# Kernel optimization log

Measured on AMD Instinct MI355X. Metric: run time of the kernel, lower is better.

The kernel has to match this reference:

```python
import jax, jax.numpy as jnp
import numpy as np

NCE_T = 0.07


def setup_inputs() -> dict:
    key = jax.random.key(0)
    k1, k2, k3 = jax.random.split(key, 3)
    features_1 = jax.random.normal(k1, (1, 20000, 256), dtype=jnp.float32)
    features_2 = jax.random.normal(k2, (1, 8192, 256), dtype=jnp.float32)
    map21 = jax.random.randint(k3, (8192,), 0, 20000, dtype=jnp.int64)
    return {"features_1": features_1, "features_2": features_2, "map21": map21}


def reference(features_1, features_2, map21):
    # squeeze leading batch dim (module assumes batch size 1)
    f1 = features_1[0]  # [N1, D]
    f2 = features_2[0]  # [P, D]  (P == nce_num_pairs == len(map21) -> arange branch)
    query = f1[map21]   # [P, D] gather
    keys = f2           # [P, D]
    # pairwise Euclidean distance via matmul trick (matches torch.cdist p=2)
    q_sq = jnp.sum(query * query, axis=-1)  # [P]
    k_sq = jnp.sum(keys * keys, axis=-1)    # [P]
    sq_dist = q_sq[:, None] + k_sq[None, :] - 2.0 * (query @ keys.T)  # [P, P]
    dist = jnp.sqrt(jnp.maximum(sq_dist, 0.0))
    logits = -dist / NCE_T
    # cross entropy with labels = arange(P): mean of -log_softmax diagonal
    logp = jax.nn.log_softmax(logits, axis=-1)
    loss = -jnp.mean(jnp.diagonal(logp))
    return loss
```

## Files before the change

kernel.cpp:

```cpp
#include <hip/hip_runtime.h>
#include <hip/hip_bf16.h>

#define PP      8192
#define DIM     256
#define DIMP    272
#define NKF     17
#define GS      (32 * DIMP)
#define NCHUNK  16
#define TCOLS   16
#define ROWBLK  256
#define NROWBLK (PP / ROWBLK)
#define TILEB   (32 * DIMP * 2)

typedef __bf16 bf16_t;
using bf16x8 = __attribute__((ext_vector_type(8))) __bf16;
using bf16x4 = __attribute__((ext_vector_type(4))) __bf16;
using f32x4  = __attribute__((ext_vector_type(4))) float;
using f32x16 = __attribute__((ext_vector_type(16))) float;

typedef __attribute__((address_space(1))) void as1_void;
typedef __attribute__((address_space(3))) void as3_void;

#define C2    20.609929155556618
#define MEXP  (-340.0f)
#define COEF  ((float)(-(C2 * 1.4142135623730951) * 8388608.0))
#define KBIAS ((float)((127.0 + 340.0) * 8388608.0))
#define LN2   0.6931471805599453f

__global__ __launch_bounds__(256) void nce_prep(
    const float* __restrict__ f1, const float* __restrict__ f2,
    const int* __restrict__ map,
    bf16_t* __restrict__ qb2, bf16_t* __restrict__ kb2,
    float* __restrict__ diag2, float* __restrict__ part_l,
    unsigned* __restrict__ cnt, float* __restrict__ out)
{
    const int tid  = threadIdx.x;
    const int wave = tid >> 6, lane = tid & 63;
    const int p    = blockIdx.x * 4 + wave;
    const int gtid = blockIdx.x * 256 + tid;

    if (gtid < PP) part_l[gtid] = 0.0f;
    if (gtid < NROWBLK) cnt[gtid] = 0u;
    if (gtid == 0) out[0] = 0.0f;

    const int idx = map[p];
    const f32x4 qv = *(const f32x4*)(f1 + (size_t)idx * DIM + lane * 4);
    const f32x4 kv = *(const f32x4*)(f2 + (size_t)p * DIM + lane * 4);

    float qs = qv[0]*qv[0] + qv[1]*qv[1] + qv[2]*qv[2] + qv[3]*qv[3];
    float ks = kv[0]*kv[0] + kv[1]*kv[1] + kv[2]*kv[2] + kv[3]*kv[3];
    const f32x4 dv = qv - kv;
    float ds = dv[0]*dv[0] + dv[1]*dv[1] + dv[2]*dv[2] + dv[3]*dv[3];

    bf16x4 qo, ko;
    #pragma unroll
    for (int i = 0; i < 4; ++i) { qo[i] = (bf16_t)qv[i]; ko[i] = (bf16_t)kv[i]; }

    const int G = p >> 5, l31 = p & 31;
    const int kk = lane >> 2, h = (lane >> 1) & 1, j0 = (lane & 1) * 4;
    const size_t base = (size_t)G * GS;
    const size_t off  = base + (size_t)(kk * 64 + h * 32 + l31) * 8 + j0;
    *(bf16x4*)(qb2 + off) = qo;
    *(bf16x4*)(kb2 + off) = ko;

    #pragma unroll
    for (int s = 32; s > 0; s >>= 1) {
        qs += __shfl_xor(qs, s);
        ks += __shfl_xor(ks, s);
        ds += __shfl_xor(ds, s);
    }

    if (lane < 4) {
        const int hh = lane & 1;
        bf16x8 v;
        #pragma unroll
        for (int i = 0; i < 8; ++i) v[i] = (bf16_t)0.0f;
        if (lane == 0) {
            const float qh = -0.5f * qs;
            const bf16_t q1 = (bf16_t)qh;
            v[0] = q1; v[1] = (bf16_t)(qh - (float)q1);
            v[2] = (bf16_t)1.0f; v[3] = (bf16_t)1.0f;
        } else if (lane == 2) {
            const float kh = -0.5f * ks;
            const bf16_t k1 = (bf16_t)kh;
            v[0] = (bf16_t)1.0f; v[1] = (bf16_t)1.0f;
            v[2] = k1; v[3] = (bf16_t)(kh - (float)k1);
        }
        bf16_t* dstp = (lane < 2) ? qb2 : kb2;
        *(bf16x8*)(dstp + base + (size_t)(1024 + hh * 32 + l31) * 8) = v;
    }
    if (lane == 0)
        diag2[p] = (float)(-C2) * __builtin_amdgcn_sqrtf(ds);
}

__device__ __forceinline__ void stage(const bf16_t* __restrict__ kb2,
                                      int Gc, int wave, int lane, char* dst)
{
    const bf16_t* src = kb2 + (size_t)Gc * GS + wave * 512 + lane * 8;
    char* d = dst + wave * 1024;
    #pragma unroll
    for (int j = 0; j < 4; ++j)
        __builtin_amdgcn_global_load_lds((const as1_void*)(src + j * 2048),
                                         (as3_void*)(d + j * 4096), 16, 0, 0);
    if (wave == 0)
        __builtin_amdgcn_global_load_lds((const as1_void*)(src + 4 * 2048),
                                         (as3_void*)(d + 4 * 4096), 16, 0, 0);
}

__global__ __launch_bounds__(256, 2) void nce_main(
    const bf16_t* __restrict__ qb2, const bf16_t* __restrict__ kb2,
    const float* __restrict__ diag2, float* __restrict__ part_l,
    unsigned* __restrict__ cnt, float* __restrict__ out)
{
    const int tid  = threadIdx.x, wave = tid >> 6, lane = tid & 63;
    const int l31  = lane & 31, h = lane >> 5;
    const int rb   = blockIdx.x;
    const int G0   = rb * 8 + wave * 2;
    const int c0g  = blockIdx.y * TCOLS;

    __shared__ __align__(16) char smem[2][TILEB];
    __shared__ int s_last;

    bf16x8 a0[NKF], a1[NKF];
    {
        const bf16_t* ap0 = qb2 + (size_t)G0 * GS + lane * 8;
        const bf16_t* ap1 = ap0 + GS;
        #pragma unroll
        for (int kk = 0; kk < NKF; ++kk) {
            a0[kk] = *(const bf16x8*)(ap0 + kk * 512);
            a1[kk] = *(const bf16x8*)(ap1 + kk * 512);
        }
    }

    float l0[16], l1[16];
    #pragma unroll
    for (int i = 0; i < 16; ++i) { l0[i] = 0.0f; l1[i] = 0.0f; }

    stage(kb2, c0g, wave, lane, smem[0]);

    for (int t = 0; t < TCOLS; ++t) {
        __syncthreads();
        if (t + 1 < TCOLS) stage(kb2, c0g + t + 1, wave, lane, smem[(t + 1) & 1]);

        const bf16_t* bp = (const bf16_t*)smem[t & 1] + lane * 8;
        f32x16 acc0 = {0,0,0,0,0,0,0,0,0,0,0,0,0,0,0,0};
        f32x16 acc1 = {0,0,0,0,0,0,0,0,0,0,0,0,0,0,0,0};
        #pragma unroll
        for (int kk = 0; kk < NKF; ++kk) {
            const bf16x8 b = *(const bf16x8*)(bp + kk * 512);
            acc0 = __builtin_amdgcn_mfma_f32_32x32x16_bf16(a0[kk], b, acc0, 0, 0, 0);
            acc1 = __builtin_amdgcn_mfma_f32_32x32x16_bf16(a1[kk], b, acc1, 0, 0, 0);
        }
        #pragma unroll
        for (int i = 0; i < 16; ++i) {
            const float t0 = __builtin_amdgcn_sqrtf(-acc0[i]);
            const float u0 = fmaxf(fmaf(t0, COEF, KBIAS), 0.0f);
            l0[i] += __uint_as_float((unsigned)u0);
            const float t1 = __builtin_amdgcn_sqrtf(-acc1[i]);
            const float u1 = fmaxf(fmaf(t1, COEF, KBIAS), 0.0f);
            l1[i] += __uint_as_float((unsigned)u1);
        }
    }

    #pragma unroll
    for (int s = 1; s < 32; s <<= 1) {
        #pragma unroll
        for (int i = 0; i < 16; ++i) {
            l0[i] += __shfl_xor(l0[i], s);
            l1[i] += __shfl_xor(l1[i], s);
        }
    }

    if (l31 == 0) {
        #pragma unroll
        for (int i = 0; i < 16; ++i) {
            const int r = (i & 3) + 8 * (i >> 2) + 4 * h;
            atomicAdd(&part_l[G0 * 32 + r], l0[i]);
            atomicAdd(&part_l[(G0 + 1) * 32 + r], l1[i]);
        }
    }

    __syncthreads();
    if (tid == 0) {
        __threadfence();
        s_last = (atomicAdd(&cnt[rb], 1u) == NCHUNK - 1) ? 1 : 0;
    }
    __syncthreads();
    if (s_last) {
        const int row = rb * ROWBLK + tid;
        const float lf = atomicAdd(&part_l[row], 0.0f);
        float v = MEXP + __builtin_amdgcn_logf(lf) - diag2[row];
        #pragma unroll
        for (int s = 1; s < 64; s <<= 1) v += __shfl_xor(v, s);
        __shared__ float red[4];
        if (lane == 0) red[wave] = v;
        __syncthreads();
        if (tid == 0)
            atomicAdd(out, (red[0] + red[1] + red[2] + red[3]) * (LN2 / (float)PP));
    }
}

extern "C" void kernel_launch(void* const* d_in, const int* in_sizes, int n_in,
                              void* d_out, int out_size, void* d_ws, size_t ws_size,
                              hipStream_t stream)
{
    const float* f1  = (const float*)d_in[0];
    const float* f2  = (const float*)d_in[1];
    const int*   map = (const int*)d_in[2];
    float* out = (float*)d_out;

    char* ws = (char*)d_ws;
    bf16_t*   qb2    = (bf16_t*)ws;
    bf16_t*   kb2    = qb2 + (size_t)256 * GS;
    float*    diag2  = (float*)(ws + 2ull * 256 * GS * sizeof(bf16_t));
    float*    part_l = diag2 + PP;
    unsigned* cnt    = (unsigned*)(part_l + PP);

    nce_prep<<<PP / 4, 256, 0, stream>>>(f1, f2, map, qb2, kb2, diag2,
                                         part_l, cnt, out);
    nce_main<<<dim3(NROWBLK, NCHUNK), 256, 0, stream>>>(qb2, kb2, diag2,
                                                        part_l, cnt, out);
}
```

Before: 118.8 us.

## Use one row group per wave with split-K accumulators and padded key groups

```diff
diff --git a/kernel.cpp b/kernel.cpp
--- a/kernel.cpp
+++ b/kernel.cpp
@@ -6,9 +6,10 @@
 #define DIMP    272
 #define NKF     17
 #define GS      (32 * DIMP)
-#define NCHUNK  16
-#define TCOLS   16
-#define ROWBLK  256
+#define NCHUNK  12
+#define TCOLS   22
+#define KGROUPS 264
+#define ROWBLK  128
 #define NROWBLK (PP / ROWBLK)
 #define TILEB   (32 * DIMP * 2)
 
@@ -42,6 +43,17 @@
     if (gtid < PP) part_l[gtid] = 0.0f;
     if (gtid < NROWBLK) cnt[gtid] = 0u;
     if (gtid == 0) out[0] = 0.0f;
+
+    if (gtid < 8 * (GS / 8)) {
+        const int g = gtid;
+        const int grp = 256 + g / (GS / 8);
+        const int c   = g % (GS / 8);
+        bf16x8 v;
+        #pragma unroll
+        for (int i = 0; i < 8; ++i) v[i] = (bf16_t)0.0f;
+        if (c >= 1024 && c < 1056) v[2] = (bf16_t)(-1.0e5f);
+        *(bf16x8*)(kb2 + (size_t)grp * GS + (size_t)c * 8) = v;
+    }
 
     const int idx = map[p];
     const f32x4 qv = *(const f32x4*)(f1 + (size_t)idx * DIM + lane * 4);
@@ -107,7 +119,7 @@
                                          (as3_void*)(d + 4 * 4096), 16, 0, 0);
 }
 
-__global__ __launch_bounds__(256, 2) void nce_main(
+__global__ __launch_bounds__(256, 3) void nce_main(
     const bf16_t* __restrict__ qb2, const bf16_t* __restrict__ kb2,
     const float* __restrict__ diag2, float* __restrict__ part_l,
     unsigned* __restrict__ cnt, float* __restrict__ out)
@@ -115,26 +127,23 @@
     const int tid  = threadIdx.x, wave = tid >> 6, lane = tid & 63;
     const int l31  = lane & 31, h = lane >> 5;
     const int rb   = blockIdx.x;
-    const int G0   = rb * 8 + wave * 2;
+    const int G    = rb * 4 + wave;
     const int c0g  = blockIdx.y * TCOLS;
 
     __shared__ __align__(16) char smem[2][TILEB];
     __shared__ int s_last;
 
-    bf16x8 a0[NKF], a1[NKF];
+    bf16x8 a[NKF];
     {
-        const bf16_t* ap0 = qb2 + (size_t)G0 * GS + lane * 8;
-        const bf16_t* ap1 = ap0 + GS;
-        #pragma unroll
-        for (int kk = 0; kk < NKF; ++kk) {
-            a0[kk] = *(const bf16x8*)(ap0 + kk * 512);
-            a1[kk] = *(const bf16x8*)(ap1 + kk * 512);
-        }
-    }
-
-    float l0[16], l1[16];
-    #pragma unroll
-    for (int i = 0; i < 16; ++i) { l0[i] = 0.0f; l1[i] = 0.0f; }
+        const bf16_t* ap = qb2 + (size_t)G * GS + lane * 8;
+        #pragma unroll
+        for (int kk = 0; kk < NKF; ++kk)
+            a[kk] = *(const bf16x8*)(ap + kk * 512);
+    }
+
+    float l[16];
+    #pragma unroll
+    for (int i = 0; i < 16; ++i) l[i] = 0.0f;
 
     stage(kb2, c0g, wave, lane, smem[0]);
 
@@ -146,37 +155,37 @@
         f32x16 acc0 = {0,0,0,0,0,0,0,0,0,0,0,0,0,0,0,0};
         f32x16 acc1 = {0,0,0,0,0,0,0,0,0,0,0,0,0,0,0,0};
         #pragma unroll
-        for (int kk = 0; kk < NKF; ++kk) {
-            const bf16x8 b = *(const bf16x8*)(bp + kk * 512);
-            acc0 = __builtin_amdgcn_mfma_f32_32x32x16_bf16(a0[kk], b, acc0, 0, 0, 0);
-            acc1 = __builtin_amdgcn_mfma_f32_32x32x16_bf16(a1[kk], b, acc1, 0, 0, 0);
-        }
+        for (int kk = 0; kk < 8; ++kk) {
+            const bf16x8 b0 = *(const bf16x8*)(bp + (2 * kk) * 512);
+            acc0 = __builtin_amdgcn_mfma_f32_32x32x16_bf16(a[2 * kk], b0, acc0, 0, 0, 0);
+            const bf16x8 b1 = *(const bf16x8*)(bp + (2 * kk + 1) * 512);
+            acc1 = __builtin_amdgcn_mfma_f32_32x32x16_bf16(a[2 * kk + 1], b1, acc1, 0, 0, 0);
+        }
+        {
+            const bf16x8 b16 = *(const bf16x8*)(bp + 16 * 512);
+            acc0 = __builtin_amdgcn_mfma_f32_32x32x16_bf16(a[16], b16, acc0, 0, 0, 0);
+        }
+
         #pragma unroll
         for (int i = 0; i < 16; ++i) {
-            const float t0 = __builtin_amdgcn_sqrtf(-acc0[i]);
+            const float s2 = acc0[i] + acc1[i];
+            const float t0 = __builtin_amdgcn_sqrtf(-s2);
             const float u0 = fmaxf(fmaf(t0, COEF, KBIAS), 0.0f);
-            l0[i] += __uint_as_float((unsigned)u0);
-            const float t1 = __builtin_amdgcn_sqrtf(-acc1[i]);
-            const float u1 = fmaxf(fmaf(t1, COEF, KBIAS), 0.0f);
-            l1[i] += __uint_as_float((unsigned)u1);
+            l[i] += __uint_as_float((unsigned)u0);
         }
     }
 
     #pragma unroll
     for (int s = 1; s < 32; s <<= 1) {
         #pragma unroll
-        for (int i = 0; i < 16; ++i) {
-            l0[i] += __shfl_xor(l0[i], s);
-            l1[i] += __shfl_xor(l1[i], s);
-        }
+        for (int i = 0; i < 16; ++i) l[i] += __shfl_xor(l[i], s);
     }
 
     if (l31 == 0) {
         #pragma unroll
         for (int i = 0; i < 16; ++i) {
             const int r = (i & 3) + 8 * (i >> 2) + 4 * h;
-            atomicAdd(&part_l[G0 * 32 + r], l0[i]);
-            atomicAdd(&part_l[(G0 + 1) * 32 + r], l1[i]);
+            atomicAdd(&part_l[G * 32 + r], l[i]);
         }
     }
 
@@ -187,9 +196,12 @@
     }
     __syncthreads();
     if (s_last) {
-        const int row = rb * ROWBLK + tid;
-        const float lf = atomicAdd(&part_l[row], 0.0f);
-        float v = MEXP + __builtin_amdgcn_logf(lf) - diag2[row];
+        float v = 0.0f;
+        if (tid < ROWBLK) {
+            const int row = rb * ROWBLK + tid;
+            const float lf = atomicAdd(&part_l[row], 0.0f);
+            v = MEXP + __builtin_amdgcn_logf(lf) - diag2[row];
+        }
         #pragma unroll
         for (int s = 1; s < 64; s <<= 1) v += __shfl_xor(v, s);
         __shared__ float red[4];
@@ -212,7 +224,7 @@
     char* ws = (char*)d_ws;
     bf16_t*   qb2    = (bf16_t*)ws;
     bf16_t*   kb2    = qb2 + (size_t)256 * GS;
-    float*    diag2  = (float*)(ws + 2ull * 256 * GS * sizeof(bf16_t));
+    float*    diag2  = (float*)(ws + ((size_t)256 + KGROUPS) * GS * sizeof(bf16_t));
     float*    part_l = diag2 + PP;
     unsigned* cnt    = (unsigned*)(part_l + PP);
 
```

Measured after the change: 128.4 us. 1.08x slower.

## Stream key tiles from global into registers and pad key groups with dummy columns

Applied to the files above, without the earlier changes.

```diff
diff --git a/kernel.cpp b/kernel.cpp
--- a/kernel.cpp
+++ b/kernel.cpp
@@ -1,25 +1,23 @@
 #include <hip/hip_runtime.h>
 #include <hip/hip_bf16.h>
 
-#define PP      8192
-#define DIM     256
-#define DIMP    272
-#define NKF     17
-#define GS      (32 * DIMP)
-#define NCHUNK  16
-#define TCOLS   16
-#define ROWBLK  256
-#define NROWBLK (PP / ROWBLK)
-#define TILEB   (32 * DIMP * 2)
+#define PP       8192
+#define DIM      256
+#define DIMP     272
+#define NKF      17
+#define GS       (32 * DIMP)
+#define NCHUNK   16
+#define TCOLS    18
+#define KGROUPS  288
+#define KGALLOC  289
+#define ROWBLK   256
+#define NROWBLK  (PP / ROWBLK)
 
 typedef __bf16 bf16_t;
 using bf16x8 = __attribute__((ext_vector_type(8))) __bf16;
 using bf16x4 = __attribute__((ext_vector_type(4))) __bf16;
 using f32x4  = __attribute__((ext_vector_type(4))) float;
 using f32x16 = __attribute__((ext_vector_type(16))) float;
-
-typedef __attribute__((address_space(1))) void as1_void;
-typedef __attribute__((address_space(3))) void as3_void;
 
 #define C2    20.609929155556618
 #define MEXP  (-340.0f)
@@ -42,6 +40,16 @@
     if (gtid < PP) part_l[gtid] = 0.0f;
     if (gtid < NROWBLK) cnt[gtid] = 0u;
     if (gtid == 0) out[0] = 0.0f;
+
+    if (gtid < 32 * (GS / 8)) {
+        const int grp = 256 + gtid / (GS / 8);
+        const int c   = gtid % (GS / 8);
+        bf16x8 v;
+        #pragma unroll
+        for (int i = 0; i < 8; ++i) v[i] = (bf16_t)0.0f;
+        if (c >= 1024 && c < 1056) v[2] = (bf16_t)(-1.0e5f);
+        *(bf16x8*)(kb2 + (size_t)grp * GS + (size_t)c * 8) = v;
+    }
 
     const int idx = map[p];
     const f32x4 qv = *(const f32x4*)(f1 + (size_t)idx * DIM + lane * 4);
@@ -93,18 +101,38 @@
         diag2[p] = (float)(-C2) * __builtin_amdgcn_sqrtf(ds);
 }
 
-__device__ __forceinline__ void stage(const bf16_t* __restrict__ kb2,
-                                      int Gc, int wave, int lane, char* dst)
-{
-    const bf16_t* src = kb2 + (size_t)Gc * GS + wave * 512 + lane * 8;
-    char* d = dst + wave * 1024;
-    #pragma unroll
-    for (int j = 0; j < 4; ++j)
-        __builtin_amdgcn_global_load_lds((const as1_void*)(src + j * 2048),
-                                         (as3_void*)(d + j * 4096), 16, 0, 0);
-    if (wave == 0)
-        __builtin_amdgcn_global_load_lds((const as1_void*)(src + 4 * 2048),
-                                         (as3_void*)(d + 4 * 4096), 16, 0, 0);
+__device__ __forceinline__ void epi(const f32x16& acc0, const f32x16& acc1,
+                                    float* l0, float* l1)
+{
+    #pragma unroll
+    for (int i = 0; i < 16; ++i) {
+        const float t0 = __builtin_amdgcn_sqrtf(-acc0[i]);
+        const float u0 = fmaxf(fmaf(t0, COEF, KBIAS), 0.0f);
+        l0[i] += __uint_as_float((unsigned)u0);
+        const float t1 = __builtin_amdgcn_sqrtf(-acc1[i]);
+        const float u1 = fmaxf(fmaf(t1, COEF, KBIAS), 0.0f);
+        l1[i] += __uint_as_float((unsigned)u1);
+    }
+}
+
+__device__ __forceinline__ void tile_body(const bf16_t*& tb,
+                                          const bf16x8* a0, const bf16x8* a1,
+                                          bf16x8* br, const bf16x8 pc,
+                                          float* l0, float* l1)
+{
+    f32x16 acc0 = {0,0,0,0,0,0,0,0,0,0,0,0,0,0,0,0};
+    f32x16 acc1 = {0,0,0,0,0,0,0,0,0,0,0,0,0,0,0,0};
+    #pragma unroll
+    for (int kk = 0; kk < 16; ++kk) {
+        const bf16x8 b = br[kk & 7];
+        acc0 = __builtin_amdgcn_mfma_f32_32x32x16_bf16(a0[kk], b, acc0, 0, 0, 0);
+        acc1 = __builtin_amdgcn_mfma_f32_32x32x16_bf16(a1[kk], b, acc1, 0, 0, 0);
+        br[kk & 7] = *(const bf16x8*)(tb + ((kk < 8) ? (kk + 8) : (kk + 9)) * 512);
+    }
+    acc0 = __builtin_amdgcn_mfma_f32_32x32x16_bf16(a0[16], pc, acc0, 0, 0, 0);
+    acc1 = __builtin_amdgcn_mfma_f32_32x32x16_bf16(a1[16], pc, acc1, 0, 0, 0);
+    epi(acc0, acc1, l0, l1);
+    tb += 17 * 512;
 }
 
 __global__ __launch_bounds__(256, 2) void nce_main(
@@ -118,8 +146,8 @@
     const int G0   = rb * 8 + wave * 2;
     const int c0g  = blockIdx.y * TCOLS;
 
-    __shared__ __align__(16) char smem[2][TILEB];
-    __shared__ int s_last;
+    __shared__ int   s_last;
+    __shared__ float red[4];
 
     bf16x8 a0[NKF], a1[NKF];
     {
@@ -136,30 +164,17 @@
     #pragma unroll
     for (int i = 0; i < 16; ++i) { l0[i] = 0.0f; l1[i] = 0.0f; }
 
-    stage(kb2, c0g, wave, lane, smem[0]);
-
-    for (int t = 0; t < TCOLS; ++t) {
-        __syncthreads();
-        if (t + 1 < TCOLS) stage(kb2, c0g + t + 1, wave, lane, smem[(t + 1) & 1]);
-
-        const bf16_t* bp = (const bf16_t*)smem[t & 1] + lane * 8;
-        f32x16 acc0 = {0,0,0,0,0,0,0,0,0,0,0,0,0,0,0,0};
-        f32x16 acc1 = {0,0,0,0,0,0,0,0,0,0,0,0,0,0,0,0};
-        #pragma unroll
-        for (int kk = 0; kk < NKF; ++kk) {
-            const bf16x8 b = *(const bf16x8*)(bp + kk * 512);
-            acc0 = __builtin_amdgcn_mfma_f32_32x32x16_bf16(a0[kk], b, acc0, 0, 0, 0);
-            acc1 = __builtin_amdgcn_mfma_f32_32x32x16_bf16(a1[kk], b, acc1, 0, 0, 0);
-        }
-        #pragma unroll
-        for (int i = 0; i < 16; ++i) {
-            const float t0 = __builtin_amdgcn_sqrtf(-acc0[i]);
-            const float u0 = fmaxf(fmaf(t0, COEF, KBIAS), 0.0f);
-            l0[i] += __uint_as_float((unsigned)u0);
-            const float t1 = __builtin_amdgcn_sqrtf(-acc1[i]);
-            const float u1 = fmaxf(fmaf(t1, COEF, KBIAS), 0.0f);
-            l1[i] += __uint_as_float((unsigned)u1);
-        }
+    const bf16_t* tb = kb2 + (size_t)c0g * GS + lane * 8;
+    bf16x8 br[8];
+    #pragma unroll
+    for (int i = 0; i < 8; ++i) br[i] = *(const bf16x8*)(tb + i * 512);
+    bf16x8 pcA = *(const bf16x8*)(tb + 16 * 512);
+
+    for (int tt = 0; tt < TCOLS; tt += 2) {
+        const bf16x8 pcB = *(const bf16x8*)(tb + 33 * 512);
+        tile_body(tb, a0, a1, br, pcA, l0, l1);
+        pcA = *(const bf16x8*)(tb + 33 * 512);
+        tile_body(tb, a0, a1, br, pcB, l0, l1);
     }
 
     #pragma unroll
@@ -192,7 +207,6 @@
         float v = MEXP + __builtin_amdgcn_logf(lf) - diag2[row];
         #pragma unroll
         for (int s = 1; s < 64; s <<= 1) v += __shfl_xor(v, s);
-        __shared__ float red[4];
         if (lane == 0) red[wave] = v;
         __syncthreads();
         if (tid == 0)
@@ -212,7 +226,7 @@
     char* ws = (char*)d_ws;
     bf16_t*   qb2    = (bf16_t*)ws;
     bf16_t*   kb2    = qb2 + (size_t)256 * GS;
-    float*    diag2  = (float*)(ws + 2ull * 256 * GS * sizeof(bf16_t));
+    float*    diag2  = (float*)(ws + ((size_t)256 + KGALLOC) * GS * sizeof(bf16_t));
     float*    part_l = diag2 + PP;
     unsigned* cnt    = (unsigned*)(part_l + PP);
 
```

Result: slower. 174.1 us (+46.6%).

## Switch to 16x16 MFMA with direct global B loads and explicit norm epilogue

Applied to the files above, without the earlier changes.

```diff
diff --git a/kernel.cpp b/kernel.cpp
--- a/kernel.cpp
+++ b/kernel.cpp
@@ -1,36 +1,31 @@
 #include <hip/hip_runtime.h>
 #include <hip/hip_bf16.h>
 
-#define PP      8192
-#define DIM     256
-#define DIMP    272
-#define NKF     17
-#define GS      (32 * DIMP)
-#define NCHUNK  16
-#define TCOLS   16
-#define ROWBLK  256
-#define NROWBLK (PP / ROWBLK)
-#define TILEB   (32 * DIMP * 2)
+#define PP       8192
+#define DIM      256
+#define GS16     4096
+#define NCHUNK   16
+#define TCOLS    32
+#define ROWBLK   256
+#define NROWBLK  (PP / ROWBLK)
 
 typedef __bf16 bf16_t;
 using bf16x8 = __attribute__((ext_vector_type(8))) __bf16;
 using bf16x4 = __attribute__((ext_vector_type(4))) __bf16;
 using f32x4  = __attribute__((ext_vector_type(4))) float;
-using f32x16 = __attribute__((ext_vector_type(16))) float;
-
-typedef __attribute__((address_space(1))) void as1_void;
-typedef __attribute__((address_space(3))) void as3_void;
 
 #define C2    20.609929155556618
 #define MEXP  (-340.0f)
-#define COEF  ((float)(-(C2 * 1.4142135623730951) * 8388608.0))
+#define COEF  ((float)(-C2 * 8388608.0))
 #define KBIAS ((float)((127.0 + 340.0) * 8388608.0))
 #define LN2   0.6931471805599453f
+
 
 __global__ __launch_bounds__(256) void nce_prep(
     const float* __restrict__ f1, const float* __restrict__ f2,
     const int* __restrict__ map,
     bf16_t* __restrict__ qb2, bf16_t* __restrict__ kb2,
+    float* __restrict__ qsq, float* __restrict__ ksq,
     float* __restrict__ diag2, float* __restrict__ part_l,
     unsigned* __restrict__ cnt, float* __restrict__ out)
 {
@@ -56,10 +51,9 @@
     #pragma unroll
     for (int i = 0; i < 4; ++i) { qo[i] = (bf16_t)qv[i]; ko[i] = (bf16_t)kv[i]; }
 
-    const int G = p >> 5, l31 = p & 31;
-    const int kk = lane >> 2, h = (lane >> 1) & 1, j0 = (lane & 1) * 4;
-    const size_t base = (size_t)G * GS;
-    const size_t off  = base + (size_t)(kk * 64 + h * 32 + l31) * 8 + j0;
+    const int G = p >> 4, l15 = p & 15;
+    const size_t off = (size_t)G * GS16 + (size_t)(lane >> 3) * 512
+                     + (size_t)(l15 + 16 * ((lane >> 1) & 3)) * 8 + (lane & 1) * 4;
     *(bf16x4*)(qb2 + off) = qo;
     *(bf16x4*)(kb2 + off) = ko;
 
@@ -69,115 +63,88 @@
         ks += __shfl_xor(ks, s);
         ds += __shfl_xor(ds, s);
     }
-
-    if (lane < 4) {
-        const int hh = lane & 1;
-        bf16x8 v;
-        #pragma unroll
-        for (int i = 0; i < 8; ++i) v[i] = (bf16_t)0.0f;
-        if (lane == 0) {
-            const float qh = -0.5f * qs;
-            const bf16_t q1 = (bf16_t)qh;
-            v[0] = q1; v[1] = (bf16_t)(qh - (float)q1);
-            v[2] = (bf16_t)1.0f; v[3] = (bf16_t)1.0f;
-        } else if (lane == 2) {
-            const float kh = -0.5f * ks;
-            const bf16_t k1 = (bf16_t)kh;
-            v[0] = (bf16_t)1.0f; v[1] = (bf16_t)1.0f;
-            v[2] = k1; v[3] = (bf16_t)(kh - (float)k1);
-        }
-        bf16_t* dstp = (lane < 2) ? qb2 : kb2;
-        *(bf16x8*)(dstp + base + (size_t)(1024 + hh * 32 + l31) * 8) = v;
+    if (lane == 0) {
+        qsq[p]   = qs;
+        ksq[p]   = ks;
+        diag2[p] = (float)(-C2) * __builtin_amdgcn_sqrtf(ds);
     }
-    if (lane == 0)
-        diag2[p] = (float)(-C2) * __builtin_amdgcn_sqrtf(ds);
-}
-
-__device__ __forceinline__ void stage(const bf16_t* __restrict__ kb2,
-                                      int Gc, int wave, int lane, char* dst)
-{
-    const bf16_t* src = kb2 + (size_t)Gc * GS + wave * 512 + lane * 8;
-    char* d = dst + wave * 1024;
-    #pragma unroll
-    for (int j = 0; j < 4; ++j)
-        __builtin_amdgcn_global_load_lds((const as1_void*)(src + j * 2048),
-                                         (as3_void*)(d + j * 4096), 16, 0, 0);
-    if (wave == 0)
-        __builtin_amdgcn_global_load_lds((const as1_void*)(src + 4 * 2048),
-                                         (as3_void*)(d + 4 * 4096), 16, 0, 0);
 }
 
 __global__ __launch_bounds__(256, 2) void nce_main(
     const bf16_t* __restrict__ qb2, const bf16_t* __restrict__ kb2,
+    const float* __restrict__ qsq, const float* __restrict__ ksq,
     const float* __restrict__ diag2, float* __restrict__ part_l,
     unsigned* __restrict__ cnt, float* __restrict__ out)
 {
     const int tid  = threadIdx.x, wave = tid >> 6, lane = tid & 63;
-    const int l31  = lane & 31, h = lane >> 5;
+    const int quad = lane >> 4, l15 = lane & 15;
     const int rb   = blockIdx.x;
-    const int G0   = rb * 8 + wave * 2;
-    const int c0g  = blockIdx.y * TCOLS;
+    const int ch   = blockIdx.y;
+    const int Gb   = rb * 16 + wave * 4;
+    const int rbase = rb * ROWBLK + wave * 64;
 
-    __shared__ __align__(16) char smem[2][TILEB];
-    __shared__ int s_last;
+    __shared__ int   s_last;
+    __shared__ float red[4];
 
-    bf16x8 a0[NKF], a1[NKF];
+    bf16x8 a[4][8];
     {
-        const bf16_t* ap0 = qb2 + (size_t)G0 * GS + lane * 8;
-        const bf16_t* ap1 = ap0 + GS;
+        const bf16_t* ap = qb2 + (size_t)Gb * GS16 + lane * 8;
         #pragma unroll
-        for (int kk = 0; kk < NKF; ++kk) {
-            a0[kk] = *(const bf16x8*)(ap0 + kk * 512);
-            a1[kk] = *(const bf16x8*)(ap1 + kk * 512);
-        }
+        for (int rg = 0; rg < 4; ++rg)
+            #pragma unroll
+            for (int f = 0; f < 8; ++f)
+                a[rg][f] = *(const bf16x8*)(ap + rg * GS16 + f * 512);
     }
 
-    float l0[16], l1[16];
+    float qs[16];
     #pragma unroll
-    for (int i = 0; i < 16; ++i) { l0[i] = 0.0f; l1[i] = 0.0f; }
+    for (int i = 0; i < 16; ++i)
+        qs[i] = qsq[rbase + (i >> 2) * 16 + quad * 4 + (i & 3)];
 
-    stage(kb2, c0g, wave, lane, smem[0]);
+    float l[16];
+    #pragma unroll
+    for (int i = 0; i < 16; ++i) l[i] = 0.0f;
+
+    const bf16_t* tb = kb2 + (size_t)ch * 32 * GS16 + lane * 8;
+    bf16x8 br[4];
+    #pragma unroll
+    for (int s = 0; s < 4; ++s) br[s] = *(const bf16x8*)(tb + s * 512);
+    const float* kqp = ksq + ch * 512 + l15;
 
     for (int t = 0; t < TCOLS; ++t) {
-        __syncthreads();
-        if (t + 1 < TCOLS) stage(kb2, c0g + t + 1, wave, lane, smem[(t + 1) & 1]);
+        const float kq = kqp[t * 16];
+        f32x4 acc0 = {0,0,0,0}, acc1 = {0,0,0,0}, acc2 = {0,0,0,0}, acc3 = {0,0,0,0};
+        #pragma unroll
+        for (int f = 0; f < 8; ++f) {
+            const bf16x8 b = br[f & 3];
+            acc0 = __builtin_amdgcn_mfma_f32_16x16x32_bf16(a[0][f], b, acc0, 0, 0, 0);
+            acc1 = __builtin_amdgcn_mfma_f32_16x16x32_bf16(a[1][f], b, acc1, 0, 0, 0);
+            acc2 = __builtin_amdgcn_mfma_f32_16x16x32_bf16(a[2][f], b, acc2, 0, 0, 0);
+            acc3 = __builtin_amdgcn_mfma_f32_16x16x32_bf16(a[3][f], b, acc3, 0, 0, 0);
+            br[f & 3] = *(const bf16x8*)(tb + (size_t)(t * 8 + f + 4) * 512);
+        }
 
-        const bf16_t* bp = (const bf16_t*)smem[t & 1] + lane * 8;
-        f32x16 acc0 = {0,0,0,0,0,0,0,0,0,0,0,0,0,0,0,0};
-        f32x16 acc1 = {0,0,0,0,0,0,0,0,0,0,0,0,0,0,0,0};
-        #pragma unroll
-        for (int kk = 0; kk < NKF; ++kk) {
-            const bf16x8 b = *(const bf16x8*)(bp + kk * 512);
-            acc0 = __builtin_amdgcn_mfma_f32_32x32x16_bf16(a0[kk], b, acc0, 0, 0, 0);
-            acc1 = __builtin_amdgcn_mfma_f32_32x32x16_bf16(a1[kk], b, acc1, 0, 0, 0);
-        }
         #pragma unroll
         for (int i = 0; i < 16; ++i) {
-            const float t0 = __builtin_amdgcn_sqrtf(-acc0[i]);
+            const float av = (i < 4) ? acc0[i & 3] : (i < 8) ? acc1[i & 3]
+                           : (i < 12) ? acc2[i & 3] : acc3[i & 3];
+            const float sq = fmaxf(fmaf(-2.0f, av, qs[i] + kq), 0.0f);
+            const float t0 = __builtin_amdgcn_sqrtf(sq);
             const float u0 = fmaxf(fmaf(t0, COEF, KBIAS), 0.0f);
-            l0[i] += __uint_as_float((unsigned)u0);
-            const float t1 = __builtin_amdgcn_sqrtf(-acc1[i]);
-            const float u1 = fmaxf(fmaf(t1, COEF, KBIAS), 0.0f);
-            l1[i] += __uint_as_float((unsigned)u1);
+            l[i] += __uint_as_float((unsigned)u0);
         }
     }
 
     #pragma unroll
-    for (int s = 1; s < 32; s <<= 1) {
+    for (int s = 1; s < 16; s <<= 1) {
         #pragma unroll
-        for (int i = 0; i < 16; ++i) {
-            l0[i] += __shfl_xor(l0[i], s);
-            l1[i] += __shfl_xor(l1[i], s);
-        }
+        for (int i = 0; i < 16; ++i) l[i] += __shfl_xor(l[i], s);
     }
 
-    if (l31 == 0) {
+    if (l15 == 0) {
         #pragma unroll
-        for (int i = 0; i < 16; ++i) {
-            const int r = (i & 3) + 8 * (i >> 2) + 4 * h;
-            atomicAdd(&part_l[G0 * 32 + r], l0[i]);
-            atomicAdd(&part_l[(G0 + 1) * 32 + r], l1[i]);
-        }
+        for (int i = 0; i < 16; ++i)
+            atomicAdd(&part_l[rbase + (i >> 2) * 16 + quad * 4 + (i & 3)], l[i]);
     }
 
     __syncthreads();
@@ -192,7 +159,6 @@
         float v = MEXP + __builtin_amdgcn_logf(lf) - diag2[row];
         #pragma unroll
         for (int s = 1; s < 64; s <<= 1) v += __shfl_xor(v, s);
-        __shared__ float red[4];
         if (lane == 0) red[wave] = v;
         __syncthreads();
         if (tid == 0)
@@ -211,13 +177,15 @@
 
     char* ws = (char*)d_ws;
     bf16_t*   qb2    = (bf16_t*)ws;
-    bf16_t*   kb2    = qb2 + (size_t)256 * GS;
-    float*    diag2  = (float*)(ws + 2ull * 256 * GS * sizeof(bf16_t));
+    bf16_t*   kb2    = qb2 + (size_t)512 * GS16;
+    float*    qsq    = (float*)(ws + (2ull * 512 * GS16 + 4096) * sizeof(bf16_t));
+    float*    ksq    = qsq + PP;
+    float*    diag2  = ksq + PP;
     float*    part_l = diag2 + PP;
     unsigned* cnt    = (unsigned*)(part_l + PP);
 
-    nce_prep<<<PP / 4, 256, 0, stream>>>(f1, f2, map, qb2, kb2, diag2,
-                                         part_l, cnt, out);
-    nce_main<<<dim3(NROWBLK, NCHUNK), 256, 0, stream>>>(qb2, kb2, diag2,
-                                                        part_l, cnt, out);
+    nce_prep<<<PP / 4, 256, 0, stream>>>(f1, f2, map, qb2, kb2, qsq, ksq,
+                                         diag2, part_l, cnt, out);
+    nce_main<<<dim3(NROWBLK, NCHUNK), 256, 0, stream>>>(qb2, kb2, qsq, ksq,
+                                                        diag2, part_l, cnt, out);
 }
```

Measured after the change: 133.7 us. 12.6% more time.
